# Performance work log

Hardware: AMD Instinct MI355X
Metric: run time of the kernel (lower is better)

Reference implementation:

```python
import jax, jax.numpy as jnp
import numpy as np

H, D, E, C, F = 12, 64, 768, 512, 3072  # heads, kq_dim, emb_dim, context_dim, mlp_hid
EPS = 1e-5
SCALE = 1.0 / float(np.sqrt(D))


def setup_inputs() -> dict:
    key = jax.random.key(0)
    ks = jax.random.split(key, 12)
    rn = lambda k, s: jax.random.normal(k, s, dtype=jnp.float32) * 0.02
    z = lambda s: jnp.zeros(s, jnp.float32)
    o = lambda s: jnp.ones(s, jnp.float32)
    return {
        "emb": jax.random.normal(ks[0], (8, 1024, E), dtype=jnp.float32),
        "context": jax.random.normal(ks[1], (8, 256, C), dtype=jnp.float32),
        # self-attention (qkv_bias=False, value_up has bias)
        "sa_wq": rn(ks[2], (E, H * D)), "sa_wk": rn(ks[3], (E, H * D)),
        "sa_wv": rn(ks[4], (E, H * D)), "sa_wo": rn(ks[5], (H * D, E)), "sa_wo_b": z((E,)),
        "sa_qn_g": o((D,)), "sa_qn_b": z((D,)), "sa_kn_g": o((D,)), "sa_kn_b": z((D,)),
        # cross-attention
        "ca_wq": rn(ks[6], (E, H * D)), "ca_wk": rn(ks[7], (C, H * D)),
        "ca_wv": rn(ks[8], (C, H * D)), "ca_wo": rn(ks[9], (H * D, E)), "ca_wo_b": z((E,)),
        "ca_qn_g": o((D,)), "ca_qn_b": z((D,)), "ca_kn_g": o((D,)), "ca_kn_b": z((D,)),
        # MLP
        "mlp_w1": rn(ks[10], (E, F)), "mlp_b1": z((F,)),
        "mlp_w2": rn(ks[11], (F, E)), "mlp_b2": z((E,)),
        # block LayerNorms
        "ln1_g": o((E,)), "ln1_b": z((E,)),
        "ln2_g": o((E,)), "ln2_b": z((E,)),
        "ln3_g": o((E,)), "ln3_b": z((E,)),
    }


def _ln(x, g, b):
    m = jnp.mean(x, axis=-1, keepdims=True)
    v = jnp.mean(jnp.square(x - m), axis=-1, keepdims=True)
    return (x - m) / jnp.sqrt(v + EPS) * g + b


def _heads(x):  # [B,S,H*D] -> [B,H,S,D]
    B, S = x.shape[:2]
    return x.reshape(B, S, H, D).transpose(0, 2, 1, 3)


def _merge(x):  # [B,H,S,D] -> [B,S,H*D]
    B, h, S, d = x.shape
    return x.transpose(0, 2, 1, 3).reshape(B, S, h * d)


def _attn(qx, kvx, wq, wk, wv, wo, wo_b, qg, qb, kg, kb):
    q = _ln(_heads(qx @ wq), qg, qb)   # per-head QK-LayerNorm
    k = _ln(_heads(kvx @ wk), kg, kb)
    v = _heads(kvx @ wv)
    a = jax.nn.softmax(jnp.einsum('bhqd,bhkd->bhqk', q, k) * SCALE, axis=-1)
    return _merge(jnp.einsum('bhqk,bhkd->bhqd', a, v)) @ wo + wo_b


def reference(emb, context,
              sa_wq, sa_wk, sa_wv, sa_wo, sa_wo_b, sa_qn_g, sa_qn_b, sa_kn_g, sa_kn_b,
              ca_wq, ca_wk, ca_wv, ca_wo, ca_wo_b, ca_qn_g, ca_qn_b, ca_kn_g, ca_kn_b,
              mlp_w1, mlp_b1, mlp_w2, mlp_b2,
              ln1_g, ln1_b, ln2_g, ln2_b, ln3_g, ln3_b):
    # MultiHeadAttention.forward returns value + emb, and the block adds emb again
    sa = _attn(emb, emb, sa_wq, sa_wk, sa_wv, sa_wo, sa_wo_b,
               sa_qn_g, sa_qn_b, sa_kn_g, sa_kn_b)
    x = _ln(sa + emb + emb, ln1_g, ln1_b)  # faithful double residual
    ca = _attn(x, context, ca_wq, ca_wk, ca_wv, ca_wo, ca_wo_b,
               ca_qn_g, ca_qn_b, ca_kn_g, ca_kn_b)
    x = _ln(x + ca, ln2_g, ln2_b)
    x = jax.nn.gelu(x @ mlp_w1 + mlp_b1, approximate=False) @ mlp_w2 + mlp_b2
    return _ln(x, ln3_g, ln3_b)  # note: no residual around MLP in the original
```

## Files before the change

kernel.cpp:

```cpp
#include <hip/hip_runtime.h>
#include <hip/hip_bf16.h>
#include <math.h>

#define NH 12
#define HD 64
#define ED 768
#define CD 512
#define FD 3072
#define BB 8
#define SS 1024
#define TT 256
#define LN_EPS 1e-5f
#define ATT_SCALE 0.125f
#define QSC_LOG2E 0.1803368801111204f
#define P_M0 11.55f
#define TOT_R 6291456

typedef __attribute__((ext_vector_type(8))) __bf16 bf16x8;
typedef __attribute__((ext_vector_type(4))) __bf16 bf16x4;
typedef __attribute__((ext_vector_type(4))) float f32x4;

typedef const __attribute__((address_space(1))) void* gas1_t;
typedef __attribute__((address_space(3))) void* las3_t;

__device__ __forceinline__ void gl16(const void* g, void* l) {
  __builtin_amdgcn_global_load_lds((gas1_t)g, (las3_t)l, 16, 0, 0);
}

__device__ __forceinline__ ushort f2bf(float f) {
  union { __bf16 b; ushort u; } c;
  c.b = (__bf16)f;
  return c.u;
}

__device__ __forceinline__ float gelu_fast(float c) {
  const float x2 = c * c;
  const float ex = __builtin_amdgcn_exp2f(c * (-2.3022084f - 0.10294325f * x2));
  return c * __builtin_amdgcn_rcpf(1.0f + ex);
}

__device__ __forceinline__ bf16x8 frag64(const ushort (*T)[64], int row, int q8) {
  return *(const bf16x8*)((const char*)T + row * 128 + ((q8 ^ (row & 7)) << 4));
}

__device__ __forceinline__ bf16x8 frag32(const ushort (*T)[32], int row, int g) {
  return *(const bf16x8*)((const char*)T + row * 64 + ((g ^ ((row >> 1) & 3)) << 4));
}

struct CvtPack {
  const float* src[12];
  ushort* dst[12];
  int kd[12];
  int nd[12];
  int off[13];
};

__global__ __launch_bounds__(256) void cvt_all(CvtPack P) {
  __shared__ float t[32][33];
  const int flat = blockIdx.x;
  int j = 0;
  while (j < 11 && flat >= P.off[j + 1]) ++j;
  const int rel = flat - P.off[j];
  if (P.nd[j] == 0) {
    const int i = rel * 256 + threadIdx.x;
    if (i < P.kd[j]) {
      float4 v = ((const float4*)P.src[j])[i];
      ((ushort4*)P.dst[j])[i] =
          make_ushort4(f2bf(v.x), f2bf(v.y), f2bf(v.z), f2bf(v.w));
    }
    return;
  }
  const int Kd = P.kd[j], Nd = P.nd[j];
  const int ntx = Nd >> 5;
  const int n0 = (rel % ntx) * 32, k0 = (rel / ntx) * 32;
  const float* W = P.src[j];
  ushort* WT = P.dst[j];
  const int tx = threadIdx.x & 31, ty = threadIdx.x >> 5;
#pragma unroll
  for (int r = 0; r < 4; ++r)
    t[ty + 8 * r][tx] = W[(size_t)(k0 + ty + 8 * r) * Nd + n0 + tx];
  __syncthreads();
#pragma unroll
  for (int r = 0; r < 4; ++r)
    WT[(size_t)(n0 + ty + 8 * r) * Kd + k0 + tx] = f2bf(t[tx][ty + 8 * r]);
}

template <int MODE, int BM>
__global__ __launch_bounds__(256, 3) void mfma_gemm(
    const ushort* __restrict__ A, const ushort* __restrict__ Wt,
    const float* __restrict__ bias, void* __restrict__ outp,
    void* __restrict__ outp2, int M, int N, int Kstride, int Klen, int sshift,
    const float* __restrict__ qg, const float* __restrict__ qb,
    const float* __restrict__ kg, const float* __restrict__ kb,
    int t_q, int t_k, int t_v) {
  constexpr int MI = BM / 32;
  __shared__ ushort As[2][BM][32];
  __shared__ ushort Bs[2][128][32];
  const int tid = threadIdx.x;
  const int m0 = blockIdx.x * BM, n0 = blockIdx.y * 128;
  const int kz = blockIdx.z;
  const ushort* Ab = A + (size_t)kz * Klen;
  const ushort* Wb = Wt + (size_t)kz * Klen;
  void* op = kz ? outp2 : outp;
  const int lane = tid & 63;
  const int wr = ((tid >> 6) >> 1) * (BM / 2), wc = ((tid >> 6) & 1) * 64;
  const int l15 = lane & 15, g = lane >> 4;
  f32x4 acc[MI][4] = {};

  auto stage = [&](int bi, int kt) {
#pragma unroll
    for (int p = 0; p < BM / 64; ++p) {
      const int fq = p * 256 + tid;
      const int row = fq >> 2, q = fq & 3;
      const int kc = 8 * (q ^ ((row >> 1) & 3));
      gl16(&Ab[(size_t)(m0 + row) * Kstride + kt + kc], (char*)As[bi] + fq * 16);
    }
#pragma unroll
    for (int p = 0; p < 2; ++p) {
      const int fq = p * 256 + tid;
      const int row = fq >> 2, q = fq & 3;
      const int kc = 8 * (q ^ ((row >> 1) & 3));
      gl16(&Wb[(size_t)(n0 + row) * Kstride + kt + kc], (char*)Bs[bi] + fq * 16);
    }
  };

  stage(0, 0);
  __syncthreads();
  int cur = 0;
  for (int kt = 0; kt < Klen; kt += 32) {
    if (kt + 32 < Klen) stage(cur ^ 1, kt + 32);
    bf16x8 af[MI], bfv[4];
#pragma unroll
    for (int i = 0; i < MI; ++i) af[i] = frag32(As[cur], wr + i * 16 + l15, g);
#pragma unroll
    for (int j = 0; j < 4; ++j) bfv[j] = frag32(Bs[cur], wc + j * 16 + l15, g);
#pragma unroll
    for (int i = 0; i < MI; ++i)
#pragma unroll
      for (int j = 0; j < 4; ++j)
        acc[i][j] = __builtin_amdgcn_mfma_f32_16x16x32_bf16(af[i], bfv[j],
                                                            acc[i][j], 0, 0, 0);
    __syncthreads();
    cur ^= 1;
  }

  if (MODE == 2) {
    ushort* out = (ushort*)op;
    const int Stok = 1 << sshift, smask = Stok - 1;
    const int ht0 = (n0 + wc) >> 6;
    const int t = ht0 / NH, h = ht0 - t * NH;
    const bool isq = (t == t_q), isk = (t == t_k);
    if (isq || isk) {
      const float* gg = isq ? qg : kg;
      const float* bb = isq ? qb : kb;
      const float osc = isq ? QSC_LOG2E : 1.0f;
      float gv[4], bv[4];
#pragma unroll
      for (int j = 0; j < 4; ++j) {
        gv[j] = gg[j * 16 + l15];
        bv[j] = bb[j * 16 + l15];
      }
#pragma unroll
      for (int i = 0; i < MI; ++i)
#pragma unroll
        for (int r = 0; r < 4; ++r) {
          float s = acc[i][0][r] + acc[i][1][r] + acc[i][2][r] + acc[i][3][r];
          float sq = acc[i][0][r] * acc[i][0][r] + acc[i][1][r] * acc[i][1][r] +
                     acc[i][2][r] * acc[i][2][r] + acc[i][3][r] * acc[i][3][r];
          s += __shfl_xor(s, 1);  sq += __shfl_xor(sq, 1);
          s += __shfl_xor(s, 2);  sq += __shfl_xor(sq, 2);
          s += __shfl_xor(s, 4);  sq += __shfl_xor(sq, 4);
          s += __shfl_xor(s, 8);  sq += __shfl_xor(sq, 8);
          const float mean = s * (1.0f / 64.0f);
          const float var = sq * (1.0f / 64.0f) - mean * mean;
          const float rs = rsqrtf(fmaxf(var, 0.0f) + LN_EPS);
#pragma unroll
          for (int j = 0; j < 4; ++j)
            acc[i][j][r] = ((acc[i][j][r] - mean) * rs * gv[j] + bv[j]) * osc;
        }
    }
    if (t == t_v) {
#pragma unroll
      for (int i = 0; i < MI; ++i) {
        const int row = m0 + wr + i * 16 + g * 4;
        const int b = row >> sshift, s2 = row & smask;
        ushort* obase =
            out + (size_t)t * TOT_R + (((size_t)b * NH + h) * 64) * Stok + s2;
#pragma unroll
        for (int j = 0; j < 4; ++j) {
          const int d = j * 16 + l15;
          ushort4 pk = make_ushort4(f2bf(acc[i][j][0]), f2bf(acc[i][j][1]),
                                    f2bf(acc[i][j][2]), f2bf(acc[i][j][3]));
          *(ushort4*)&obase[(size_t)d * Stok] = pk;
        }
      }
    } else {
#pragma unroll
      for (int i = 0; i < MI; ++i)
#pragma unroll
        for (int r = 0; r < 4; ++r) {
          const int row = m0 + wr + i * 16 + g * 4 + r;
          const int b = row >> sshift, s2 = row & smask;
          ushort* orow =
              out + (size_t)t * TOT_R + (((size_t)b * NH + h) * Stok + s2) * 64;
#pragma unroll
          for (int j = 0; j < 4; ++j) orow[j * 16 + l15] = f2bf(acc[i][j][r]);
        }
    }
  } else {
#pragma unroll
    for (int i = 0; i < MI; ++i) {
#pragma unroll
      for (int j = 0; j < 4; ++j) {
        const int gc = n0 + wc + j * 16 + l15;
        const float bv = bias ? bias[gc] : 0.0f;
#pragma unroll
        for (int r = 0; r < 4; ++r) {
          const int row = m0 + wr + i * 16 + g * 4 + r;
          float c = acc[i][j][r] + bv;
          if (MODE == 1) {
            c = gelu_fast(c);
            ((ushort*)op)[(size_t)row * N + gc] = f2bf(c);
          } else {
            ((float*)op)[(size_t)row * N + gc] = c;
          }
        }
      }
    }
  }
}

__global__ __launch_bounds__(512) void flash_mfma(
    const ushort* __restrict__ Q, const ushort* __restrict__ K,
    const ushort* __restrict__ V, ushort* __restrict__ out, int Tkv) {
  __shared__ ushort Ks[2][64][64];
  __shared__ ushort Vt[2][80][64];
  __shared__ ushort Ps[8][16][64];
  const int bh = blockIdx.x;
  const int b = bh / NH, h = bh % NH;
  const int qt = blockIdx.y;
  const int tid = threadIdx.x;
  const int w = tid >> 6, lane = tid & 63;
  const int l15 = lane & 15, g = lane >> 4;
  const int srow = tid >> 3;
  const int q8s = tid & 7;
  const int skc = 8 * (q8s ^ (srow & 7));
  const int kperm = 4 * (srow & 15) + (srow >> 4);

  const ushort* Qb = Q + ((size_t)bh * SS + qt * 256) * 64;
  const ushort* Kb = K + (size_t)bh * Tkv * 64;
  const ushort* Vb = V + (size_t)bh * Tkv * 64;

  gl16(&Kb[(size_t)kperm * 64 + skc], (char*)Ks[0] + tid * 16);
  gl16(&Vb[(size_t)srow * Tkv + skc], (char*)Vt[0] + tid * 16);

  if (tid < 256) {
    const int bi = tid >> 7, rq = tid & 127;
    const uint4 ov = make_uint4(0x3F803F80u, 0x3F803F80u, 0x3F803F80u, 0x3F803F80u);
    *(uint4*)((char*)Vt[bi] + (64 + (rq >> 3)) * 128 + ((rq & 7) << 4)) = ov;
  }

  const ushort* qr0 = Qb + (w * 32 + l15) * 64;
  const bf16x8 qf00 = *(const bf16x8*)&qr0[g * 8];
  const bf16x8 qf01 = *(const bf16x8*)&qr0[32 + g * 8];
  const bf16x8 qf10 = *(const bf16x8*)&qr0[16 * 64 + g * 8];
  const bf16x8 qf11 = *(const bf16x8*)&qr0[16 * 64 + 32 + g * 8];
  __syncthreads();

  f32x4 oa[2][5] = {};
  const int pwofs = ((((l15 >> 1) ^ ((g * 4) & 7)) << 4) | ((l15 & 1) << 3));

  const int nch = Tkv >> 6;
  int cur = 0;
  for (int ci = 0; ci < nch; ++ci) {
    if (ci + 1 < nch) {
      const int cnx = (ci + 1) << 6;
      const int nxt = cur ^ 1;
      gl16(&Kb[(size_t)(cnx + kperm) * 64 + skc], (char*)Ks[nxt] + tid * 16);
      gl16(&Vb[(size_t)srow * Tkv + cnx + skc], (char*)Vt[nxt] + tid * 16);
    }

    f32x4 s[2][4] = {};
    __builtin_amdgcn_s_setprio(1);
#pragma unroll
    for (int kb = 0; kb < 4; ++kb) {
      bf16x8 kf0 = frag64(Ks[cur], kb * 16 + l15, g);
      bf16x8 kf1 = frag64(Ks[cur], kb * 16 + l15, 4 + g);
      s[0][kb] = __builtin_amdgcn_mfma_f32_16x16x32_bf16(qf00, kf0, s[0][kb], 0, 0, 0);
      s[0][kb] = __builtin_amdgcn_mfma_f32_16x16x32_bf16(qf01, kf1, s[0][kb], 0, 0, 0);
      s[1][kb] = __builtin_amdgcn_mfma_f32_16x16x32_bf16(qf10, kf0, s[1][kb], 0, 0, 0);
      s[1][kb] = __builtin_amdgcn_mfma_f32_16x16x32_bf16(qf11, kf1, s[1][kb], 0, 0, 0);
    }
    __builtin_amdgcn_s_setprio(0);

    bf16x8 pfr[2][2];
#pragma unroll
    for (int sub = 0; sub < 2; ++sub) {
#pragma unroll
      for (int r = 0; r < 4; ++r) {
        bf16x4 pk;
#pragma unroll
        for (int kbv = 0; kbv < 4; ++kbv)
          pk[kbv] = (__bf16)__builtin_amdgcn_exp2f(s[sub][kbv][r] - P_M0);
        *(bf16x4*)((char*)Ps[w] + (g * 4 + r) * 128 + (pwofs ^ ((r & 7) << 4))) = pk;
      }
      pfr[sub][0] = frag64(Ps[w], l15, g);
      pfr[sub][1] = frag64(Ps[w], l15, 4 + g);
    }

    __builtin_amdgcn_s_setprio(1);
#pragma unroll
    for (int jd = 0; jd < 5; ++jd) {
      const int d = jd * 16 + l15;
      bf16x8 vf0 = frag64(Vt[cur], d, g);
      bf16x8 vf1 = frag64(Vt[cur], d, 4 + g);
      oa[0][jd] = __builtin_amdgcn_mfma_f32_16x16x32_bf16(pfr[0][0], vf0, oa[0][jd], 0, 0, 0);
      oa[0][jd] = __builtin_amdgcn_mfma_f32_16x16x32_bf16(pfr[0][1], vf1, oa[0][jd], 0, 0, 0);
      oa[1][jd] = __builtin_amdgcn_mfma_f32_16x16x32_bf16(pfr[1][0], vf0, oa[1][jd], 0, 0, 0);
      oa[1][jd] = __builtin_amdgcn_mfma_f32_16x16x32_bf16(pfr[1][1], vf1, oa[1][jd], 0, 0, 0);
    }
    __builtin_amdgcn_s_setprio(0);

    __syncthreads();
    cur ^= 1;
  }

#pragma unroll
  for (int sub = 0; sub < 2; ++sub)
#pragma unroll
    for (int r = 0; r < 4; ++r) {
      const int row = qt * 256 + w * 32 + sub * 16 + g * 4 + r;
      const float inv = 1.0f / oa[sub][4][r];
#pragma unroll
      for (int jd = 0; jd < 4; ++jd)
        out[((size_t)b * SS + row) * ED + h * 64 + jd * 16 + l15] =
            f2bf(oa[sub][jd][r] * inv);
    }
}

__global__ __launch_bounds__(256) void add_ln(
    const float* __restrict__ a1, const float* __restrict__ a2,
    const float* __restrict__ bsrc, float alpha,
    const float* __restrict__ cbias,
    const float* __restrict__ g, const float* __restrict__ bt,
    float* __restrict__ outf, ushort* __restrict__ outb) {
  const int row = blockIdx.x * 4 + (threadIdx.x >> 6);
  const int lane = threadIdx.x & 63;
  const size_t base = (size_t)row * ED;
  float4 x[3];
#pragma unroll
  for (int p = 0; p < 3; ++p) {
    const int idx = p * 256 + lane * 4;
    x[p] = *(const float4*)&a1[base + idx];
    if (a2) {
      float4 v = *(const float4*)&a2[base + idx];
      x[p].x += v.x; x[p].y += v.y; x[p].z += v.z; x[p].w += v.w;
    }
    if (bsrc) {
      float4 bv = *(const float4*)&bsrc[base + idx];
      x[p].x += alpha * bv.x;
      x[p].y += alpha * bv.y;
      x[p].z += alpha * bv.z;
      x[p].w += alpha * bv.w;
    }
    if (cbias) {
      float4 cv = *(const float4*)&cbias[idx];
      x[p].x += cv.x; x[p].y += cv.y; x[p].z += cv.z; x[p].w += cv.w;
    }
  }
  float s = 0.f;
#pragma unroll
  for (int p = 0; p < 3; ++p) s += x[p].x + x[p].y + x[p].z + x[p].w;
  for (int off = 32; off; off >>= 1) s += __shfl_xor(s, off);
  const float mean = s * (1.0f / 768.0f);
  float v = 0.f;
#pragma unroll
  for (int p = 0; p < 3; ++p) {
    float d0 = x[p].x - mean, d1 = x[p].y - mean;
    float d2 = x[p].z - mean, d3 = x[p].w - mean;
    v += d0 * d0 + d1 * d1 + d2 * d2 + d3 * d3;
  }
  for (int off = 32; off; off >>= 1) v += __shfl_xor(v, off);
  const float rs = rsqrtf(v * (1.0f / 768.0f) + LN_EPS);
#pragma unroll
  for (int p = 0; p < 3; ++p) {
    const int idx = p * 256 + lane * 4;
    const float4 gv = *(const float4*)&g[idx];
    const float4 bb = *(const float4*)&bt[idx];
    const float y0 = (x[p].x - mean) * rs * gv.x + bb.x;
    const float y1 = (x[p].y - mean) * rs * gv.y + bb.y;
    const float y2 = (x[p].z - mean) * rs * gv.z + bb.z;
    const float y3 = (x[p].w - mean) * rs * gv.w + bb.w;
    if (outf) *(float4*)&outf[base + idx] = make_float4(y0, y1, y2, y3);
    if (outb)
      *(ushort4*)&outb[base + idx] =
          make_ushort4(f2bf(y0), f2bf(y1), f2bf(y2), f2bf(y3));
  }
}

extern "C" void kernel_launch(void* const* d_in, const int* in_sizes, int n_in,
                              void* d_out, int out_size, void* d_ws,
                              size_t ws_size, hipStream_t stream) {
  (void)in_sizes; (void)n_in; (void)out_size; (void)ws_size;
  const float* emb     = (const float*)d_in[0];
  const float* context = (const float*)d_in[1];
  const float* sa_wq = (const float*)d_in[2];
  const float* sa_wk = (const float*)d_in[3];
  const float* sa_wv = (const float*)d_in[4];
  const float* sa_wo = (const float*)d_in[5];
  const float* sa_wo_b = (const float*)d_in[6];
  const float* sa_qn_g = (const float*)d_in[7];
  const float* sa_qn_b = (const float*)d_in[8];
  const float* sa_kn_g = (const float*)d_in[9];
  const float* sa_kn_b = (const float*)d_in[10];
  const float* ca_wq = (const float*)d_in[11];
  const float* ca_wk = (const float*)d_in[12];
  const float* ca_wv = (const float*)d_in[13];
  const float* ca_wo = (const float*)d_in[14];
  const float* ca_wo_b = (const float*)d_in[15];
  const float* ca_qn_g = (const float*)d_in[16];
  const float* ca_qn_b = (const float*)d_in[17];
  const float* ca_kn_g = (const float*)d_in[18];
  const float* ca_kn_b = (const float*)d_in[19];
  const float* mlp_w1 = (const float*)d_in[20];
  const float* mlp_b1 = (const float*)d_in[21];
  const float* mlp_w2 = (const float*)d_in[22];
  const float* mlp_b2 = (const float*)d_in[23];
  const float* ln1_g = (const float*)d_in[24];
  const float* ln1_b = (const float*)d_in[25];
  const float* ln2_g = (const float*)d_in[26];
  const float* ln2_b = (const float*)d_in[27];
  const float* ln3_g = (const float*)d_in[28];
  const float* ln3_b = (const float*)d_in[29];
  float* out = (float*)d_out;

  const size_t R = TOT_R;
  ushort* U = (ushort*)d_ws;
  ushort* Qh  = U;
  ushort* Kh  = U + R;
  ushort* Vh  = U + 2 * R;
  ushort* SH1 = U + 3 * R;
  ushort* SH2 = U + 4 * R;
  ushort* WB  = U + 5 * R;
  float*  X1  = (float*)(U + 5 * R + 9043968);
  float*  P2  = X1 + R;
  float*  WOt = (float*)Qh;
  ushort* Hb  = Qh;

  ushort* w_saqkv = WB;
  ushort* w_sao   = WB + 1769472;
  ushort* w_caq   = WB + 2359296;
  ushort* w_cakv  = WB + 2949120;
  ushort* w_cao   = WB + 3735552;
  ushort* w_m1    = WB + 4325376;
  ushort* w_m2    = WB + 6684672;

  dim3 blk(256);

  CvtPack P;
  const float* srcs[12] = {sa_wq, sa_wk, sa_wv, sa_wo, ca_wq, ca_wk, ca_wv,
                           ca_wo, mlp_w1, mlp_w2, emb, context};
  ushort* dsts[12] = {w_saqkv, w_saqkv + 589824, w_saqkv + 1179648, w_sao,
                      w_caq, w_cakv, w_cakv + 393216, w_cao, w_m1, w_m2,
                      SH1, SH2};
  const int kds[12] = {ED, ED, ED, ED, ED, CD, CD, ED, ED, FD,
                       1572864, 262144};
  const int nds[12] = {ED, ED, ED, ED, ED, ED, ED, ED, FD, ED, 0, 0};
  int off = 0;
  for (int j = 0; j < 12; ++j) {
    P.src[j] = srcs[j]; P.dst[j] = dsts[j]; P.kd[j] = kds[j]; P.nd[j] = nds[j];
    P.off[j] = off;
    off += nds[j] ? (nds[j] >> 5) * (kds[j] >> 5) : (kds[j] + 255) >> 8;
  }
  P.off[12] = off;
  cvt_all<<<dim3(off), blk, 0, stream>>>(P);

  mfma_gemm<2, 128><<<dim3(64, 18, 1), blk, 0, stream>>>(
      SH1, w_saqkv, nullptr, Qh, nullptr, 8192, 2304, ED, ED, 10,
      sa_qn_g, sa_qn_b, sa_kn_g, sa_kn_b, 0, 1, 2);
  flash_mfma<<<dim3(96, 4), dim3(512), 0, stream>>>(Qh, Kh, Vh, SH1, SS);
  mfma_gemm<0, 128><<<dim3(64, 6, 2), blk, 0, stream>>>(
      SH1, w_sao, nullptr, X1, P2, 8192, ED, ED, ED / 2, 0,
      nullptr, nullptr, nullptr, nullptr, -1, -1, -1);
  add_ln<<<dim3(2048), blk, 0, stream>>>(X1, P2, emb, 2.0f, sa_wo_b,
                                         ln1_g, ln1_b, X1, SH1);

  mfma_gemm<2, 128><<<dim3(64, 6, 1), blk, 0, stream>>>(
      SH1, w_caq, nullptr, Qh, nullptr, 8192, ED, ED, ED, 10,
      ca_qn_g, ca_qn_b, nullptr, nullptr, 0, -1, -1);
  mfma_gemm<2, 64><<<dim3(32, 12, 1), blk, 0, stream>>>(
      SH2, w_cakv, nullptr, Kh, nullptr, 2048, 1536, CD, CD, 8,
      nullptr, nullptr, ca_kn_g, ca_kn_b, -1, 0, 1);
  flash_mfma<<<dim3(96, 4), dim3(512), 0, stream>>>(Qh, Kh, Vh, SH1, TT);
  mfma_gemm<0, 128><<<dim3(64, 6, 2), blk, 0, stream>>>(
      SH1, w_cao, nullptr, WOt, P2, 8192, ED, ED, ED / 2, 0,
      nullptr, nullptr, nullptr, nullptr, -1, -1, -1);
  add_ln<<<dim3(2048), blk, 0, stream>>>(WOt, P2, X1, 1.0f, ca_wo_b,
                                         ln2_g, ln2_b, nullptr, SH2);

  mfma_gemm<1, 128><<<dim3(64, 24, 1), blk, 0, stream>>>(
      SH2, w_m1, mlp_b1, Hb, nullptr, 8192, FD, ED, ED, 0,
      nullptr, nullptr, nullptr, nullptr, -1, -1, -1);
  mfma_gemm<0, 128><<<dim3(64, 6, 2), blk, 0, stream>>>(
      Hb, w_m2, nullptr, X1, P2, 8192, ED, FD, FD / 2, 0,
      nullptr, nullptr, nullptr, nullptr, -1, -1, -1);
  add_ln<<<dim3(2048), blk, 0, stream>>>(X1, P2, nullptr, 0.0f, mlp_b2,
                                         ln3_g, ln3_b, out, nullptr);
}
```

Baseline: 349.3 us.

## Triple-buffer GEMM LDS staging with explicit vmcnt waits

Turns the MFMA GEMM's double-buffered async global-to-LDS staging into a three-stage ring that keeps two K-tiles in flight. Explicit s_waitcnt vmcnt values replace __syncthreads, so each step waits only for the oldest tile. This hides more global-load latency behind MFMA work. In exchange it uses 1.5x the LDS, which may lower occupancy under launch_bounds(256,3), and the hand-counted waits are fragile if the number of loads issued per stage changes.

```diff
diff --git a/kernel.cpp b/kernel.cpp
--- a/kernel.cpp
+++ b/kernel.cpp
@@ -27,6 +27,15 @@
   __builtin_amdgcn_global_load_lds((gas1_t)g, (las3_t)l, 16, 0, 0);
 }
 
+template <int N>
+__device__ __forceinline__ void vm_wait() {
+  if constexpr (N == 0) asm volatile("s_waitcnt vmcnt(0)" ::: "memory");
+  else if constexpr (N == 3) asm volatile("s_waitcnt vmcnt(3)" ::: "memory");
+  else if constexpr (N == 4) asm volatile("s_waitcnt vmcnt(4)" ::: "memory");
+  else if constexpr (N == 6) asm volatile("s_waitcnt vmcnt(6)" ::: "memory");
+  else if constexpr (N == 8) asm volatile("s_waitcnt vmcnt(8)" ::: "memory");
+}
+
 __device__ __forceinline__ ushort f2bf(float f) {
   union { __bf16 b; ushort u; } c;
   c.b = (__bf16)f;
@@ -94,8 +103,9 @@
     const float* __restrict__ kg, const float* __restrict__ kb,
     int t_q, int t_k, int t_v) {
   constexpr int MI = BM / 32;
-  __shared__ ushort As[2][BM][32];
-  __shared__ ushort Bs[2][128][32];
+  constexpr int LPS = BM / 64 + 2;
+  __shared__ ushort As[3][BM][32];
+  __shared__ ushort Bs[3][128][32];
   const int tid = threadIdx.x;
   const int m0 = blockIdx.x * BM, n0 = blockIdx.y * 128;
   const int kz = blockIdx.z;
@@ -124,24 +134,35 @@
     }
   };
 
+  const int nst = Klen >> 5;
   stage(0, 0);
-  __syncthreads();
-  int cur = 0;
-  for (int kt = 0; kt < Klen; kt += 32) {
-    if (kt + 32 < Klen) stage(cur ^ 1, kt + 32);
+  stage(1, 32);
+  int cb = 0;
+  for (int step = 0; step < nst; ++step) {
+    if (step + 2 < nst) {
+      int pb = cb + 2; if (pb >= 3) pb -= 3;
+      stage(pb, (step + 2) * 32);
+    }
+    const int rem = nst - 1 - step;
+    if (rem >= 2) vm_wait<2 * LPS>();
+    else if (rem == 1) vm_wait<LPS>();
+    else vm_wait<0>();
+    __builtin_amdgcn_s_barrier();
+    asm volatile("" ::: "memory");
     bf16x8 af[MI], bfv[4];
 #pragma unroll
-    for (int i = 0; i < MI; ++i) af[i] = frag32(As[cur], wr + i * 16 + l15, g);
-#pragma unroll
-    for (int j = 0; j < 4; ++j) bfv[j] = frag32(Bs[cur], wc + j * 16 + l15, g);
+    for (int i = 0; i < MI; ++i) af[i] = frag32(As[cb], wr + i * 16 + l15, g);
+#pragma unroll
+    for (int j = 0; j < 4; ++j) bfv[j] = frag32(Bs[cb], wc + j * 16 + l15, g);
 #pragma unroll
     for (int i = 0; i < MI; ++i)
 #pragma unroll
       for (int j = 0; j < 4; ++j)
         acc[i][j] = __builtin_amdgcn_mfma_f32_16x16x32_bf16(af[i], bfv[j],
                                                             acc[i][j], 0, 0, 0);
-    __syncthreads();
-    cur ^= 1;
+    asm volatile("" ::: "memory");
+    __builtin_amdgcn_s_barrier();
+    if (++cb >= 3) cb = 0;
   }
 
   if (MODE == 2) {
```

After: 344.7 us. Within noise of the previous version (-1.3%).
